# Optimization experiments

Hardware: AMD Instinct MI355X
Metric: run time of the kernel (lower is better)

Reference implementation:

```python
import jax, jax.numpy as jnp
import numpy as np

EPS = 1e-8  # torch F.cosine_similarity default eps


def setup_inputs() -> dict:
    key = jax.random.key(0)
    k1, k2, k3 = jax.random.split(key, 3)
    B, S, D, O, W = 256, 10, 4096, 4096, 5
    x = jax.random.normal(k1, (B, S, D), dtype=jnp.float32)
    # Conv1d params: weight [out, in, kernel], bias [out]
    conv_w = jax.random.normal(k2, (O, D, W), dtype=jnp.float32) * (1.0 / np.sqrt(D * W))
    conv_b = jax.random.normal(k3, (O,), dtype=jnp.float32) * 0.01
    return {"x": x, "conv_w": conv_w, "conv_b": conv_b}


def reference(x, conv_w, conv_b):
    B, S, D = x.shape
    # central frame: original code uses index S//2 + 1 (faithful off-by-one)
    central = x[:, S // 2 + 1, :]  # [B, D]
    dots = jnp.einsum('bsd,bd->bs', x, central)  # [B, S]
    xn = jnp.maximum(jnp.linalg.norm(x, axis=-1), EPS)      # [B, S]
    cn = jnp.maximum(jnp.linalg.norm(central, axis=-1), EPS)  # [B]
    cos = dots / (xn * cn[:, None])  # [B, S]
    # original multiplies by RAW (unnormalized) cosine weights
    xw = x * cos[:, :, None]  # [B, S, D]
    # conv1d over time: [B, D, S] -> [B, O, S-W+1]
    y = jax.lax.conv_general_dilated(
        jnp.transpose(xw, (0, 2, 1)), conv_w,
        window_strides=(1,), padding='VALID',
        dimension_numbers=('NCH', 'OIH', 'NCH'))
    y = y + conv_b[None, :, None]
    return jnp.mean(y, axis=-1)  # [B, O]
```

## Files before the change

### kernel.cpp

```cpp
#include <hip/hip_runtime.h>


#define BDIM 256
#define SEQ 10
#define DDIM 4096
#define ODIM 4096
#define WDIM 5
#define GK 20480
#define SPLITS 8
#define KSPLIT (GK / SPLITS)
#define BK 64
#define KITERS (KSPLIT / BK)

typedef __bf16 bf16x8 __attribute__((ext_vector_type(8)));
typedef float f32x4 __attribute__((ext_vector_type(4)));

__device__ __forceinline__ unsigned short f2bf(float f) {
    union { float f; unsigned v; } c; c.f = f;
    unsigned r = c.v + 0x7FFFu + ((c.v >> 16) & 1u);
    return (unsigned short)(r >> 16);
}
__device__ __forceinline__ void async16(void* lds, const void* g) {
    __builtin_amdgcn_global_load_lds(
        (const __attribute__((address_space(1))) void*)g,
        (__attribute__((address_space(3))) void*)lds, 16, 0, 0);
}

__global__ __launch_bounds__(256) void cosp_kernel(const float* __restrict__ x,
                                                   unsigned short* __restrict__ P)
{
    const int b = blockIdx.x;
    const int tid = threadIdx.x;
    const float* xb = x + (size_t)b * SEQ * DDIM;

    float dot[SEQ], sq[SEQ];
#pragma unroll
    for (int s = 0; s < SEQ; ++s) { dot[s] = 0.f; sq[s] = 0.f; }

    for (int base = 0; base < DDIM; base += 1024) {
        const int d = base + tid * 4;
        const f32x4 c4 = *(const f32x4*)(xb + 6 * DDIM + d);
#pragma unroll
        for (int s = 0; s < SEQ; ++s) {
            const f32x4 v4 = *(const f32x4*)(xb + s * DDIM + d);
            dot[s] += v4[0] * c4[0] + v4[1] * c4[1] + v4[2] * c4[2] + v4[3] * c4[3];
            sq[s]  += v4[0] * v4[0] + v4[1] * v4[1] + v4[2] * v4[2] + v4[3] * v4[3];
        }
    }
#pragma unroll
    for (int s = 0; s < SEQ; ++s) {
#pragma unroll
        for (int off = 32; off > 0; off >>= 1) {
            dot[s] += __shfl_down(dot[s], off, 64);
            sq[s]  += __shfl_down(sq[s], off, 64);
        }
    }
    __shared__ float red[4][2 * SEQ];
    __shared__ float cs[SEQ];
    const int wave = tid >> 6, lane = tid & 63;
    if (lane == 0) {
#pragma unroll
        for (int s = 0; s < SEQ; ++s) { red[wave][s] = dot[s]; red[wave][SEQ + s] = sq[s]; }
    }
    __syncthreads();
    if (tid == 0) {
        const float S6 = red[0][SEQ + 6] + red[1][SEQ + 6] + red[2][SEQ + 6] + red[3][SEQ + 6];
        const float cn = fmaxf(sqrtf(S6), 1e-8f);
#pragma unroll
        for (int s = 0; s < SEQ; ++s) {
            const float Dv = red[0][s] + red[1][s] + red[2][s] + red[3][s];
            const float Sv = red[0][SEQ + s] + red[1][SEQ + s] + red[2][SEQ + s] + red[3][SEQ + s];
            cs[s] = Dv / (fmaxf(sqrtf(Sv), 1e-8f) * cn);
        }
    }
    __syncthreads();

    float csr[SEQ];
#pragma unroll
    for (int s = 0; s < SEQ; ++s) csr[s] = cs[s];

    for (int chunk = 3; chunk >= 0; --chunk) {
        const int d0 = chunk * 1024 + tid * 4;
        const float* xd = xb + d0;
        float sc[SEQ][4];
#pragma unroll
        for (int s = 0; s < SEQ; ++s) {
            const f32x4 v4 = *(const f32x4*)(xd + s * DDIM);
            sc[s][0] = v4[0] * csr[s]; sc[s][1] = v4[1] * csr[s];
            sc[s][2] = v4[2] * csr[s]; sc[s][3] = v4[3] * csr[s];
        }
        __attribute__((aligned(16))) unsigned short o[20];
#pragma unroll
        for (int w = 0; w < WDIM; ++w) {
#pragma unroll
            for (int j = 0; j < 4; ++j) {
                const float p = sc[w][j] + sc[w + 1][j] + sc[w + 2][j] +
                                sc[w + 3][j] + sc[w + 4][j] + sc[w + 5][j];
                o[j * WDIM + w] = f2bf(p);
            }
        }
        unsigned short* dst = P + ((size_t)b * DDIM + d0) * WDIM;
#pragma unroll
        for (int q = 0; q < 5; ++q)
            *(uint2*)(dst + q * 4) = *(const uint2*)(o + q * 4);
    }
}

__global__ __launch_bounds__(256, 2) void gemm_splitk_kernel(const unsigned short* __restrict__ A,
                                                             const float* __restrict__ W,
                                                             float* __restrict__ Cpart)
{
    const int bid = blockIdx.x;
    const int sp = bid & 7;
    const int nt = bid >> 3;
    const int tid = threadIdx.x;
    const int lane = tid & 63;
    const int wave = tid >> 6;

    __shared__ __align__(16) unsigned short lds_a[2][256 * BK];
    __shared__ __align__(16) unsigned short lds_w[2][64 * BK];

    f32x4 acc[4][4];
#pragma unroll
    for (int i = 0; i < 4; ++i)
#pragma unroll
        for (int j = 0; j < 4; ++j)
            acc[i][j] = (f32x4){0.f, 0.f, 0.f, 0.f};

    const int s_arow = tid >> 3;
    const int s_aoct = tid & 7;

    const int s_wrow = tid >> 2;
    const float* wsrc = W + ((size_t)(nt * 64 + s_wrow)) * GK + (tid & 3) * 16;
    const int wo0 = (((tid & 3) * 2)     ^ (s_wrow & 7)) * 8;
    const int wo1 = (((tid & 3) * 2 + 1) ^ (s_wrow & 7)) * 8;

    const int fm = lane & 15;
    const int fg = lane >> 4;
    int aoff[2][4], woff[2][4];
#pragma unroll
    for (int i = 0; i < 4; ++i) {
        const int ra = wave * 64 + i * 16 + fm;
        const int rw = i * 16 + fm;
#pragma unroll
        for (int kh = 0; kh < 2; ++kh) {
            aoff[kh][i] = ra * BK + (((kh * 4 + fg) ^ (ra & 7)) * 8);
            woff[kh][i] = rw * BK + (((kh * 4 + fg) ^ (rw & 7)) * 8);
        }
    }

#define STAGE_A(buf, kk)                                                        \
    _Pragma("unroll")                                                           \
    for (int q = 0; q < 8; ++q) {                                               \
        const int row_ = q * 32 + s_arow;                                       \
        const unsigned short* src_ =                                            \
            A + (size_t)row_ * GK + (kk) + ((s_aoct ^ (row_ & 7)) * 8);         \
        async16((char*)&lds_a[buf][0] + q * 4096 + tid * 16, src_);             \
    }

#define LOAD_W(kk)                                                              \
    w0 = *(const f32x4*)(wsrc + (kk));                                          \
    w1 = *(const f32x4*)(wsrc + (kk) + 4);                                      \
    w2 = *(const f32x4*)(wsrc + (kk) + 8);                                      \
    w3 = *(const f32x4*)(wsrc + (kk) + 12);

#define WRITE_W(buf)                                                            \
    {                                                                           \
        bf16x8 lo_, hi_;                                                        \
        _Pragma("unroll")                                                       \
        for (int e = 0; e < 4; ++e) {                                           \
            lo_[e] = (__bf16)w0[e]; lo_[4 + e] = (__bf16)w1[e];                 \
            hi_[e] = (__bf16)w2[e]; hi_[4 + e] = (__bf16)w3[e];                 \
        }                                                                       \
        *(bf16x8*)&lds_w[buf][s_wrow * BK + wo0] = lo_;                         \
        *(bf16x8*)&lds_w[buf][s_wrow * BK + wo1] = hi_;                         \
    }

#define COMPUTE(buf)                                                            \
    _Pragma("unroll")                                                           \
    for (int kh = 0; kh < 2; ++kh) {                                            \
        bf16x8 af[4], wf[4];                                                    \
        _Pragma("unroll")                                                       \
        for (int i = 0; i < 4; ++i) af[i] = *(const bf16x8*)&lds_a[buf][aoff[kh][i]]; \
        _Pragma("unroll")                                                       \
        for (int j = 0; j < 4; ++j) wf[j] = *(const bf16x8*)&lds_w[buf][woff[kh][j]]; \
        _Pragma("unroll")                                                       \
        for (int i = 0; i < 4; ++i)                                             \
            _Pragma("unroll")                                                   \
            for (int j = 0; j < 4; ++j)                                         \
                acc[i][j] = __builtin_amdgcn_mfma_f32_16x16x32_bf16(            \
                    af[i], wf[j], acc[i][j], 0, 0, 0);                          \
    }

    int k0 = sp * KSPLIT;
    f32x4 w0, w1, w2, w3;

    STAGE_A(0, k0);
    LOAD_W(k0);
    WRITE_W(0);
    __syncthreads();

    for (int it = 0; it < KITERS - 1; ++it) {
        const int cur = it & 1, nxt = cur ^ 1;
        STAGE_A(nxt, k0 + BK);
        LOAD_W(k0 + BK);
        COMPUTE(cur);
        WRITE_W(nxt);
        __syncthreads();
        k0 += BK;
    }
    COMPUTE((KITERS - 1) & 1);

    float* Cp = Cpart + (size_t)sp * (BDIM * ODIM);
    const int mbase = wave * 64 + fg * 4;
    const int nbase = nt * 64 + fm;
#pragma unroll
    for (int i = 0; i < 4; ++i)
#pragma unroll
        for (int j = 0; j < 4; ++j) {
            const int n = nbase + j * 16;
#pragma unroll
            for (int r = 0; r < 4; ++r) {
                const int m = mbase + i * 16 + r;
                Cp[(size_t)m * ODIM + n] = acc[i][j][r];
            }
        }
#undef STAGE_A
#undef LOAD_W
#undef WRITE_W
#undef COMPUTE
}

__global__ __launch_bounds__(256) void reduce_kernel(const float* __restrict__ part,
                                                     const float* __restrict__ bias,
                                                     float* __restrict__ out)
{
    const int idx = (blockIdx.x * 256 + threadIdx.x) * 4;
    f32x4 s = (f32x4){0.f, 0.f, 0.f, 0.f};
#pragma unroll
    for (int sp = 0; sp < SPLITS; ++sp) {
        const f32x4 v = *(const f32x4*)(part + (size_t)sp * (BDIM * ODIM) + idx);
        s[0] += v[0]; s[1] += v[1]; s[2] += v[2]; s[3] += v[3];
    }
    const int n = idx & (ODIM - 1);
    const f32x4 b4 = *(const f32x4*)(bias + n);
    const float inv6 = 1.0f / 6.0f;
    f32x4 o;
#pragma unroll
    for (int e = 0; e < 4; ++e) o[e] = s[e] * inv6 + b4[e];
    *(f32x4*)(out + idx) = o;
}

extern "C" void kernel_launch(void* const* d_in, const int* in_sizes, int n_in,
                              void* d_out, int out_size, void* d_ws, size_t ws_size,
                              hipStream_t stream) {
    const float* x  = (const float*)d_in[0];
    const float* cw = (const float*)d_in[1];
    const float* cb = (const float*)d_in[2];
    float* out = (float*)d_out;

    char* ws = (char*)d_ws;
    unsigned short* P = (unsigned short*)(ws + 16384);
    float* parts = (float*)(ws + 16384 + (size_t)BDIM * GK * 2);

    hipLaunchKernelGGL(cosp_kernel,        dim3(256),  dim3(256), 0, stream, x, P);
    hipLaunchKernelGGL(gemm_splitk_kernel, dim3(512),  dim3(256), 0, stream, P, cw, parts);
    hipLaunchKernelGGL(reduce_kernel,      dim3(1024), dim3(256), 0, stream, parts, cb, out);
}
```

Baseline: 501.3 us.

## Prefetch weight tiles two stages ahead with explicit vmcnt waits

The GEMM main loop now keeps two register sets for the fp32 weight tile, so global loads for weights run two K-steps ahead instead of one. The loop is unrolled by two, and __syncthreads is replaced with hand-placed s_waitcnt vmcnt/lgkmcnt plus s_barrier and sched_barrier fences. This should hide more global-load latency behind MFMA work and avoid the full-drain waits the compiler puts in at __syncthreads. The cost is extra VGPR pressure from the second set of weight registers, and hardcoded vmcnt counts that silently depend on how many loads each macro issues.

Result: no change. 493.3 us (-1.6%).

```diff
diff --git a/kernel.cpp b/kernel.cpp
--- a/kernel.cpp
+++ b/kernel.cpp
@@ -26,6 +26,11 @@
         (__attribute__((address_space(3))) void*)lds, 16, 0, 0);
 }
 
+#define VMWAIT(n) asm volatile("s_waitcnt vmcnt(" #n ")" ::: "memory")
+#define LGKM0()   asm volatile("s_waitcnt lgkmcnt(0)" ::: "memory")
+#define SBAR()    __builtin_amdgcn_s_barrier()
+#define SCHED0()  __builtin_amdgcn_sched_barrier(0)
+
 __global__ __launch_bounds__(256) void cosp_kernel(const float* __restrict__ x,
                                                    unsigned short* __restrict__ P)
 {
@@ -158,19 +163,19 @@
         async16((char*)&lds_a[buf][0] + q * 4096 + tid * 16, src_);             \
     }
 
-#define LOAD_W(kk)                                                              \
-    w0 = *(const f32x4*)(wsrc + (kk));                                          \
-    w1 = *(const f32x4*)(wsrc + (kk) + 4);                                      \
-    w2 = *(const f32x4*)(wsrc + (kk) + 8);                                      \
-    w3 = *(const f32x4*)(wsrc + (kk) + 12);
-
-#define WRITE_W(buf)                                                            \
+#define LOAD_W(R0, R1, R2, R3, kk)                                              \
+    R0 = *(const f32x4*)(wsrc + (kk));                                          \
+    R1 = *(const f32x4*)(wsrc + (kk) + 4);                                      \
+    R2 = *(const f32x4*)(wsrc + (kk) + 8);                                      \
+    R3 = *(const f32x4*)(wsrc + (kk) + 12);
+
+#define WRITE_W(buf, R0, R1, R2, R3)                                            \
     {                                                                           \
         bf16x8 lo_, hi_;                                                        \
         _Pragma("unroll")                                                       \
         for (int e = 0; e < 4; ++e) {                                           \
-            lo_[e] = (__bf16)w0[e]; lo_[4 + e] = (__bf16)w1[e];                 \
-            hi_[e] = (__bf16)w2[e]; hi_[4 + e] = (__bf16)w3[e];                 \
+            lo_[e] = (__bf16)R0[e]; lo_[4 + e] = (__bf16)R1[e];                 \
+            hi_[e] = (__bf16)R2[e]; hi_[4 + e] = (__bf16)R3[e];                 \
         }                                                                       \
         *(bf16x8*)&lds_w[buf][s_wrow * BK + wo0] = lo_;                         \
         *(bf16x8*)&lds_w[buf][s_wrow * BK + wo1] = hi_;                         \
@@ -192,24 +197,47 @@
                     af[i], wf[j], acc[i][j], 0, 0, 0);                          \
     }
 
-    int k0 = sp * KSPLIT;
-    f32x4 w0, w1, w2, w3;
-
-    STAGE_A(0, k0);
-    LOAD_W(k0);
-    WRITE_W(0);
-    __syncthreads();
-
-    for (int it = 0; it < KITERS - 1; ++it) {
-        const int cur = it & 1, nxt = cur ^ 1;
-        STAGE_A(nxt, k0 + BK);
-        LOAD_W(k0 + BK);
-        COMPUTE(cur);
-        WRITE_W(nxt);
-        __syncthreads();
-        k0 += BK;
-    }
-    COMPUTE((KITERS - 1) & 1);
+    const int ksp = sp * KSPLIT;
+    f32x4 wA0, wA1, wA2, wA3;
+    f32x4 wB0, wB1, wB2, wB3;
+
+    LOAD_W(wA0, wA1, wA2, wA3, ksp);
+    STAGE_A(0, ksp);
+    VMWAIT(8); SCHED0();
+    WRITE_W(0, wA0, wA1, wA2, wA3);
+    LOAD_W(wB0, wB1, wB2, wB3, ksp + BK);
+    VMWAIT(4); SCHED0();
+    LGKM0();
+    SBAR(); SCHED0();
+
+    int kbase = ksp;
+    for (int tt = 0; tt < (KITERS - 2) / 2; ++tt) {
+        SCHED0();
+        STAGE_A(1, kbase + BK);
+        LOAD_W(wA0, wA1, wA2, wA3, kbase + 2 * BK);
+        VMWAIT(12); SCHED0();
+        COMPUTE(0);
+        WRITE_W(1, wB0, wB1, wB2, wB3);
+        LGKM0();
+        SBAR(); SCHED0();
+        kbase += BK;
+        STAGE_A(0, kbase + BK);
+        LOAD_W(wB0, wB1, wB2, wB3, kbase + 2 * BK);
+        VMWAIT(12); SCHED0();
+        COMPUTE(1);
+        WRITE_W(0, wA0, wA1, wA2, wA3);
+        LGKM0();
+        SBAR(); SCHED0();
+        kbase += BK;
+    }
+    STAGE_A(1, kbase + BK);
+    VMWAIT(8); SCHED0();
+    COMPUTE(0);
+    WRITE_W(1, wB0, wB1, wB2, wB3);
+    LGKM0();
+    SBAR(); SCHED0();
+    VMWAIT(0); SCHED0();
+    COMPUTE(1);
 
     float* Cp = Cpart + (size_t)sp * (BDIM * ODIM);
     const int mbase = wave * 64 + fg * 4;
```
